# Performance work log

Measured on AMD Instinct MI355X. Metric: run time of the kernel, lower is better.

Reference implementation:

```python
import jax, jax.numpy as jnp
import numpy as np


def gcn_layer(x, src, dst, deg_inv_sqrt, W, b):
    # PyG GCNConv: h = X W; out[i] = sum_{j->i} norm(j,i) * h[j] + deg_i^{-1} * h[i] + b
    n = x.shape[0]
    h = x @ W                                   # [N, out]
    norm = deg_inv_sqrt[src] * deg_inv_sqrt[dst]  # [E]
    msg = h[src] * norm[:, None]                # [E, out]
    agg = jax.ops.segment_sum(msg, dst, num_segments=n)
    # self-loop contribution (added loops with norm = deg_i^{-1})
    agg = agg + h * (deg_inv_sqrt * deg_inv_sqrt)[:, None]
    return agg + b


def setup_inputs() -> dict:
    key = jax.random.key(0)
    k1, k2, k3, k4, k5, k6 = jax.random.split(key, 6)
    N, E, IN, HID, OUT = 50000, 800000, 128, 128, 64
    x = jax.random.normal(k1, (N, IN), dtype=jnp.float32)
    edge_index = jax.random.randint(k2, (2, E), 0, N, dtype=jnp.int64)
    # glorot-ish init for weights, zeros-ish bias
    W1 = jax.random.normal(k3, (IN, HID), dtype=jnp.float32) * (1.0 / np.sqrt(IN))
    b1 = jax.random.normal(k4, (HID,), dtype=jnp.float32) * 0.01
    W2 = jax.random.normal(k5, (HID, OUT), dtype=jnp.float32) * (1.0 / np.sqrt(HID))
    b2 = jax.random.normal(k6, (OUT,), dtype=jnp.float32) * 0.01
    return {"x": x, "edge_index": edge_index, "W1": W1, "b1": b1, "W2": W2, "b2": b2}


def reference(x, edge_index, W1, b1, W2, b2):
    n = x.shape[0]
    src, dst = edge_index[0], edge_index[1]
    # degree with self-loops (PyG computes degree on the dst/col index)
    deg = jax.ops.segment_sum(jnp.ones_like(dst, dtype=x.dtype), dst, num_segments=n) + 1.0
    deg_inv_sqrt = jax.lax.rsqrt(deg)
    h = gcn_layer(x, src, dst, deg_inv_sqrt, W1, b1)
    h = jax.nn.relu(h)
    # F.dropout with training=False is identity (module evaluated in eval mode)
    out = gcn_layer(h, src, dst, deg_inv_sqrt, W2, b2)
    return out
```

## Files before the change

kernel.cpp:

```cpp
#include <hip/hip_runtime.h>
#include <stdint.h>

typedef __attribute__((ext_vector_type(8))) short short8;
typedef __attribute__((ext_vector_type(4))) float floatx4;

static inline size_t align256(size_t x) { return (x + 255) & ~size_t(255); }

__device__ __forceinline__ unsigned short f2bf(float f) {
    unsigned u = __float_as_uint(f);
    u += 0x7fff + ((u >> 16) & 1);
    return (unsigned short)(u >> 16);
}
__device__ __forceinline__ unsigned pack_bf16(float a, float b) {
    return (unsigned)f2bf(a) | ((unsigned)f2bf(b) << 16);
}
__device__ __forceinline__ float bf_lo(unsigned u) { return __uint_as_float(u << 16); }
__device__ __forceinline__ float bf_hi(unsigned u) { return __uint_as_float(u & 0xffff0000u); }

#define BSHIFT 7
#define NBMAX 1024
#define CH 2048
#define SCAP 3072

__device__ __forceinline__ bool detect_i32(const void* eidx, int E, int t) {
    const long long* e64 = (const long long*)eidx;
    int nchk = E < 256 ? E : 256;
    long long v = e64[t % nchk];
    int bad = (v < 0 || v > 0x7fffffffLL) ? 1 : 0;
    return __syncthreads_or(bad) != 0;
}

__global__ __launch_bounds__(256) void k_hist(const void* __restrict__ eidx, int E,
        int* __restrict__ chist, int NB, int NC,
        const float* __restrict__ W1, const float* __restrict__ W2,
        unsigned short* __restrict__ w1t, unsigned short* __restrict__ w2t,
        int K1, int M1, int K2, int M2) {
    __shared__ int hist[NBMAX];
    const int t = threadIdx.x, B = blockIdx.x;
    if (B < NC) {
        const int e0 = B * CH;
        const int e1 = (e0 + CH < E) ? e0 + CH : E;
        const bool i32 = detect_i32(eidx, E, t);
        const int* e32 = (const int*)eidx;
        const long long* e64 = (const long long*)eidx;
        for (int b0 = 0; b0 < NB; b0 += NBMAX) {
            int bw = (NB - b0 < NBMAX) ? NB - b0 : NBMAX;
            for (int i = t; i < bw; i += 256) hist[i] = 0;
            __syncthreads();
            for (int e = e0 + t; e < e1; e += 256) {
                int d = i32 ? e32[(size_t)E + e] : (int)e64[(size_t)E + e];
                int b = (d >> BSHIFT) - b0;
                if (b >= 0 && b < bw) atomicAdd(&hist[b], 1);
            }
            __syncthreads();
            for (int i = t; i < bw; i += 256) chist[(size_t)(b0 + i) * NC + B] = hist[i];
            __syncthreads();
        }
    } else if (B == NC) {
        for (int j = t; j < K1 * M1; j += 256) {
            int k = j / M1, n = j % M1;
            w1t[(size_t)n * K1 + k] = f2bf(W1[j]);
        }
    } else if (B == NC + 1) {
        for (int j = t; j < K2 * M2; j += 256) {
            int k = j / M2, n = j % M2;
            w2t[(size_t)n * K2 + k] = f2bf(W2[j]);
        }
    }
}

__global__ __launch_bounds__(256) void k_btot(const int* __restrict__ chist,
                                              int* __restrict__ btot, int NB, int NC) {
    int b = blockIdx.x * 4 + (threadIdx.x >> 6);
    if (b >= NB) return;
    int lane = threadIdx.x & 63;
    const int* row = chist + (size_t)b * NC;
    int v = 0;
    for (int i = lane; i < NC; i += 64) v += row[i];
    #pragma unroll
    for (int off = 32; off >= 1; off >>= 1) v += __shfl_xor(v, off, 64);
    if (lane == 0) btot[b] = v;
}

__global__ __launch_bounds__(1024) void k_bscan(const int* __restrict__ btot,
                                                int* __restrict__ bbase,
                                                int* __restrict__ rs_final,
                                                int NB, int N) {
    __shared__ int swt[16];
    const int t = threadIdx.x, lane = t & 63, w = t >> 6;
    int carry = 0;
    for (int base = 0; base < NB; base += 1024) {
        int i = base + t;
        int v = (i < NB) ? btot[i] : 0;
        int incl = v;
        #pragma unroll
        for (int off = 1; off < 64; off <<= 1) {
            int nbr = __shfl_up(incl, off, 64);
            if (lane >= off) incl += nbr;
        }
        if (lane == 63) swt[w] = incl;
        __syncthreads();
        int woff = 0;
        for (int j = 0; j < w; ++j) woff += swt[j];
        if (i < NB) bbase[i] = carry + woff + incl - v;
        int tot = 0;
        for (int j = 0; j < 16; ++j) tot += swt[j];
        carry += tot;
        __syncthreads();
    }
    if (t == 0) { bbase[NB] = carry; rs_final[N] = carry; }
}

__global__ __launch_bounds__(256) void k_hscan2(int* __restrict__ chist,
                                                const int* __restrict__ bbase,
                                                int NB, int NC) {
    int b = blockIdx.x * 4 + (threadIdx.x >> 6);
    if (b >= NB) return;
    int lane = threadIdx.x & 63;
    int* row = chist + (size_t)b * NC;
    int carry = bbase[b];
    for (int base = 0; base < NC; base += 64) {
        int i = base + lane;
        int v = (i < NC) ? row[i] : 0;
        int incl = v;
        #pragma unroll
        for (int off = 1; off < 64; off <<= 1) {
            int nbr = __shfl_up(incl, off, 64);
            if (lane >= off) incl += nbr;
        }
        if (i < NC) row[i] = carry + incl - v;
        carry += __shfl(incl, 63, 64);
    }
}

__global__ __launch_bounds__(256) void k_bfill(const void* __restrict__ eidx, int E,
                                               const int* __restrict__ chist,
                                               unsigned* __restrict__ bbuf, int NB, int NC) {
    __shared__ int rank[NBMAX];
    __shared__ int base[NBMAX];
    const int t = threadIdx.x, c = blockIdx.x;
    const int e0 = c * CH;
    const int e1 = (e0 + CH < E) ? e0 + CH : E;
    const bool i32 = detect_i32(eidx, E, t);
    const int* e32 = (const int*)eidx;
    const long long* e64 = (const long long*)eidx;
    for (int b0 = 0; b0 < NB; b0 += NBMAX) {
        int bw = (NB - b0 < NBMAX) ? NB - b0 : NBMAX;
        for (int i = t; i < bw; i += 256) {
            rank[i] = 0;
            base[i] = chist[(size_t)(b0 + i) * NC + c];
        }
        __syncthreads();
        for (int e = e0 + t; e < e1; e += 256) {
            int s, d;
            if (i32) { s = e32[e]; d = e32[(size_t)E + e]; }
            else     { s = (int)e64[e]; d = (int)e64[(size_t)E + e]; }
            int b = (d >> BSHIFT) - b0;
            if (b >= 0 && b < bw) {
                int slot = base[b] + atomicAdd(&rank[b], 1);
                bbuf[slot] = ((unsigned)(d & 127) << 25) | (unsigned)s;
            }
        }
        __syncthreads();
    }
}

__global__ __launch_bounds__(256) void k_sort(const unsigned* __restrict__ bbuf,
                                              const int* __restrict__ bbase,
                                              int* __restrict__ rs_final,
                                              float* __restrict__ dinv,
                                              int* __restrict__ esrc, int N) {
    __shared__ int hist[128];
    __shared__ int off[128];
    __shared__ int srcbuf[SCAP];
    const int b = blockIdx.x, t = threadIdx.x;
    const int node0 = b << BSHIFT;
    const int nloc = (N - node0 < 128) ? N - node0 : 128;
    const int s0 = bbase[b], s1 = bbase[b + 1];
    const int cnt = s1 - s0;
    if (t < 128) hist[t] = 0;
    __syncthreads();
    for (int i = s0 + t; i < s1; i += 256)
        atomicAdd(&hist[bbuf[i] >> 25], 1);
    __syncthreads();
    if (t < 64) {
        int carry = 0;
        #pragma unroll
        for (int base = 0; base < 128; base += 64) {
            int v = hist[base + t];
            int incl = v;
            #pragma unroll
            for (int o = 1; o < 64; o <<= 1) {
                int nbr = __shfl_up(incl, o, 64);
                if (t >= o) incl += nbr;
            }
            off[base + t] = carry + incl - v;
            carry += __shfl(incl, 63, 64);
        }
    }
    __syncthreads();
    if (t < nloc) {
        rs_final[node0 + t] = s0 + off[t];
        dinv[node0 + t] = rsqrtf((float)hist[t] + 1.0f);
    }
    __syncthreads();
    if (t < 128) hist[t] = 0;
    __syncthreads();
    if (cnt <= SCAP) {
        for (int i = s0 + t; i < s1; i += 256) {
            unsigned sd = bbuf[i];
            int lo = sd >> 25;
            int r = atomicAdd(&hist[lo], 1);
            srcbuf[off[lo] + r] = (int)(sd & 0x1ffffffu);
        }
        __syncthreads();
        for (int i = t; i < cnt; i += 256) esrc[s0 + i] = srcbuf[i];
    } else {
        for (int i = s0 + t; i < s1; i += 256) {
            unsigned sd = bbuf[i];
            int lo = sd >> 25;
            int r = atomicAdd(&hist[lo], 1);
            esrc[s0 + off[lo] + r] = (int)(sd & 0x1ffffffu);
        }
    }
}

template<int BN, bool AF32>
__global__ __launch_bounds__(256, 3) void k_gemm(
        const void* __restrict__ Av, const unsigned short* __restrict__ Bt,
        const float* __restrict__ dinv, unsigned short* __restrict__ C,
        int N, int M) {
    constexpr int LD = 136;
    __shared__ unsigned short As[64 * LD];
    __shared__ unsigned short Bs[BN * LD];
    const int tid = threadIdx.x;
    const int wave = tid >> 6, lane = tid & 63;
    const int q = lane >> 4, tm = lane & 15;
    const int row0 = blockIdx.x * 64;

    {
        const uint4* Bg = (const uint4*)Bt;
        #pragma unroll
        for (int it = 0; it < BN / 16; ++it) {
            int i = tid + it * 256;
            int r = i >> 4, o = i & 15;
            *(uint4*)&Bs[r * LD + o * 8] = Bg[(size_t)r * 16 + o];
        }
    }
    if (AF32) {
        const float4* Ag = (const float4*)Av;
        #pragma unroll
        for (int it = 0; it < 8; ++it) {
            int i = tid + it * 256;
            int r = i >> 5, o = i & 31;
            int row = row0 + r;
            float4 v = make_float4(0.f, 0.f, 0.f, 0.f);
            if (row < N) v = Ag[(size_t)row * 32 + o];
            uint2 pk;
            pk.x = pack_bf16(v.x, v.y);
            pk.y = pack_bf16(v.z, v.w);
            *(uint2*)&As[r * LD + o * 4] = pk;
        }
    } else {
        const uint4* Ag = (const uint4*)Av;
        #pragma unroll
        for (int it = 0; it < 4; ++it) {
            int i = tid + it * 256;
            int r = i >> 4, o = i & 15;
            int row = row0 + r;
            uint4 v = make_uint4(0, 0, 0, 0);
            if (row < N) v = Ag[(size_t)row * 16 + o];
            *(uint4*)&As[r * LD + o * 8] = v;
        }
    }
    __syncthreads();

    constexpr int NG = BN / 16;
    floatx4 acc[NG];
    #pragma unroll
    for (int g = 0; g < NG; ++g) acc[g] = (floatx4){0.f, 0.f, 0.f, 0.f};

    const int arow = wave * 16 + tm;
    #pragma unroll
    for (int kc = 0; kc < 4; ++kc) {
        short8 af = *(const short8*)&As[arow * LD + kc * 32 + q * 8];
        #pragma unroll
        for (int g = 0; g < NG; ++g) {
            short8 bf = *(const short8*)&Bs[(g * 16 + tm) * LD + kc * 32 + q * 8];
            acc[g] = __builtin_amdgcn_mfma_f32_16x16x32_bf16(af, bf, acc[g], 0, 0, 0);
        }
    }

    float dv[4];
    #pragma unroll
    for (int r = 0; r < 4; ++r) {
        int row = row0 + wave * 16 + q * 4 + r;
        dv[r] = (row < N) ? dinv[row] : 0.f;
    }
    #pragma unroll
    for (int g = 0; g < NG; ++g) {
        #pragma unroll
        for (int r = 0; r < 4; ++r) {
            int row = row0 + wave * 16 + q * 4 + r;
            if (row < N) C[(size_t)row * M + g * 16 + tm] = f2bf(dv[r] * acc[g][r]);
        }
    }
}

__global__ __launch_bounds__(256) void k_agg128(const unsigned* __restrict__ Hb,
        const float* __restrict__ dinv, const int* __restrict__ rs,
        const int* __restrict__ esrc, const float* __restrict__ bias,
        unsigned* __restrict__ out, int N) {
    int wid = (blockIdx.x * 256 + threadIdx.x) >> 6;
    if (wid >= N) return;
    int l = threadIdx.x & 63;
    float di = dinv[wid];
    unsigned a = Hb[(size_t)wid * 64 + l];
    float accx = bf_lo(a), accy = bf_hi(a);
    int k = rs[wid], kend = rs[wid + 1];
    for (; k + 8 <= kend; k += 8) {
        int s[8];
        #pragma unroll
        for (int j = 0; j < 8; ++j) s[j] = esrc[k + j];
        unsigned g[8];
        #pragma unroll
        for (int j = 0; j < 8; ++j) g[j] = Hb[(size_t)s[j] * 64 + l];
        #pragma unroll
        for (int j = 0; j < 8; ++j) { accx += bf_lo(g[j]); accy += bf_hi(g[j]); }
    }
    if (k + 4 <= kend) {
        int s[4];
        #pragma unroll
        for (int j = 0; j < 4; ++j) s[j] = esrc[k + j];
        unsigned g[4];
        #pragma unroll
        for (int j = 0; j < 4; ++j) g[j] = Hb[(size_t)s[j] * 64 + l];
        #pragma unroll
        for (int j = 0; j < 4; ++j) { accx += bf_lo(g[j]); accy += bf_hi(g[j]); }
        k += 4;
    }
    for (; k < kend; ++k) {
        unsigned g = Hb[(size_t)esrc[k] * 64 + l];
        accx += bf_lo(g); accy += bf_hi(g);
    }
    float2 b = ((const float2*)bias)[l];
    float ox = fmaxf(fmaf(di, accx, b.x), 0.f);
    float oy = fmaxf(fmaf(di, accy, b.y), 0.f);
    out[(size_t)wid * 64 + l] = pack_bf16(ox, oy);
}

__global__ __launch_bounds__(256) void k_agg64(const unsigned short* __restrict__ Hb,
        const float* __restrict__ dinv, const int* __restrict__ rs,
        const int* __restrict__ esrc, const float* __restrict__ bias,
        float* __restrict__ out, int N) {
    int wid = (blockIdx.x * 256 + threadIdx.x) >> 6;
    if (wid >= N) return;
    int l = threadIdx.x & 63;
    float di = dinv[wid];
    float acc = __uint_as_float((unsigned)Hb[(size_t)wid * 64 + l] << 16);
    int k = rs[wid], kend = rs[wid + 1];
    for (; k + 8 <= kend; k += 8) {
        int s[8];
        #pragma unroll
        for (int j = 0; j < 8; ++j) s[j] = esrc[k + j];
        unsigned short g[8];
        #pragma unroll
        for (int j = 0; j < 8; ++j) g[j] = Hb[(size_t)s[j] * 64 + l];
        #pragma unroll
        for (int j = 0; j < 8; ++j) acc += __uint_as_float((unsigned)g[j] << 16);
    }
    if (k + 4 <= kend) {
        int s[4];
        #pragma unroll
        for (int j = 0; j < 4; ++j) s[j] = esrc[k + j];
        unsigned short g[4];
        #pragma unroll
        for (int j = 0; j < 4; ++j) g[j] = Hb[(size_t)s[j] * 64 + l];
        #pragma unroll
        for (int j = 0; j < 4; ++j) acc += __uint_as_float((unsigned)g[j] << 16);
        k += 4;
    }
    for (; k < kend; ++k)
        acc += __uint_as_float((unsigned)Hb[(size_t)esrc[k] * 64 + l] << 16);
    out[(size_t)wid * 64 + l] = fmaf(di, acc, bias[l]);
}

extern "C" void kernel_launch(void* const* d_in, const int* in_sizes, int n_in,
                              void* d_out, int out_size, void* d_ws, size_t ws_size,
                              hipStream_t stream) {
    const float* x  = (const float*)d_in[0];
    const void*  ei = d_in[1];
    const float* W1 = (const float*)d_in[2];
    const float* b1 = (const float*)d_in[3];
    const float* W2 = (const float*)d_in[4];
    const float* b2 = (const float*)d_in[5];

    int HID = in_sizes[3];
    int IN  = in_sizes[2] / HID;
    int OUT = in_sizes[4] / HID;
    int N   = in_sizes[0] / IN;
    int E   = in_sizes[1] / 2;
    int NB  = (N + 127) >> BSHIFT;
    int NC  = (E + CH - 1) / CH;

    char* p = (char*)d_ws;
    int* chist     = (int*)p;   p += align256((size_t)NB * NC * 4);
    int* btot      = (int*)p;   p += align256((size_t)NB * 4);
    int* bbase     = (int*)p;   p += align256((size_t)(NB + 1) * 4);
    int* rs_final  = (int*)p;   p += align256((size_t)(N + 1) * 4);
    int* esrc      = (int*)p;   p += align256((size_t)E * 4);
    float* dinv    = (float*)p; p += align256((size_t)N * 4);
    unsigned short* w1t = (unsigned short*)p; p += align256((size_t)HID * IN * 2);
    unsigned short* w2t = (unsigned short*)p; p += align256((size_t)OUT * HID * 2);
    size_t hb_bytes = (size_t)N * HID * 2, bbuf_bytes = (size_t)E * 4;
    unsigned* bbuf = (unsigned*)p;
    unsigned short* hb = (unsigned short*)p;
    p += align256(hb_bytes > bbuf_bytes ? hb_bytes : bbuf_bytes);
    unsigned short* h1b = (unsigned short*)p; p += align256((size_t)N * HID * 2);
    unsigned short* h2b = (unsigned short*)p; p += align256((size_t)N * OUT * 2);

    k_hist<<<NC + 2, 256, 0, stream>>>(ei, E, chist, NB, NC,
                                       W1, W2, w1t, w2t, IN, HID, HID, OUT);
    k_btot<<<(NB + 3) / 4, 256, 0, stream>>>(chist, btot, NB, NC);
    k_bscan<<<1, 1024, 0, stream>>>(btot, bbase, rs_final, NB, N);
    k_hscan2<<<(NB + 3) / 4, 256, 0, stream>>>(chist, bbase, NB, NC);
    k_bfill<<<NC, 256, 0, stream>>>(ei, E, chist, bbuf, NB, NC);
    k_sort<<<NB, 256, 0, stream>>>(bbuf, bbase, rs_final, dinv, esrc, N);

    k_gemm<128, true><<<(N + 63) / 64, 256, 0, stream>>>(x, w1t, dinv, hb, N, HID);
    k_agg128<<<(N + 3) / 4, 256, 0, stream>>>((unsigned*)hb, dinv, rs_final, esrc, b1,
                                              (unsigned*)h1b, N);

    k_gemm<64, false><<<(N + 63) / 64, 256, 0, stream>>>(h1b, w2t, dinv, h2b, N, OUT);
    k_agg64<<<(N + 3) / 4, 256, 0, stream>>>(h2b, dinv, rs_final, esrc, b2, (float*)d_out, N);
}
```

Before: 208.8 us.

## Vectorize aggregation gathers with 16-byte loads and split edges across lane groups

Both aggregation kernels now have each lane load a uint4 (8 bf16 values) per neighbor row. Each wave is split into groups of lanes that handle different edges at the same time, and the partial sums are combined with xor-shuffle reductions at the end. Edge indices are read cooperatively, 64 at a time, and handed out with shuffles instead of per-lane scalar loads. This aims to cut gather instruction count and raise memory-level parallelism, at the cost of extra shuffle reductions and idle lanes in the final write.

```diff
diff --git a/kernel.cpp b/kernel.cpp
--- a/kernel.cpp
+++ b/kernel.cpp
@@ -307,82 +307,153 @@
     }
 }
 
-__global__ __launch_bounds__(256) void k_agg128(const unsigned* __restrict__ Hb,
+#define ACC8(v) do { \
+    a0 += bf_lo((v).x); a1 += bf_hi((v).x); \
+    a2 += bf_lo((v).y); a3 += bf_hi((v).y); \
+    a4 += bf_lo((v).z); a5 += bf_hi((v).z); \
+    a6 += bf_lo((v).w); a7 += bf_hi((v).w); } while (0)
+
+__global__ __launch_bounds__(256) void k_agg128(const uint4* __restrict__ H4,
         const float* __restrict__ dinv, const int* __restrict__ rs,
         const int* __restrict__ esrc, const float* __restrict__ bias,
-        unsigned* __restrict__ out, int N) {
+        uint4* __restrict__ out, int N) {
     int wid = (blockIdx.x * 256 + threadIdx.x) >> 6;
     if (wid >= N) return;
     int l = threadIdx.x & 63;
-    float di = dinv[wid];
-    unsigned a = Hb[(size_t)wid * 64 + l];
-    float accx = bf_lo(a), accy = bf_hi(a);
-    int k = rs[wid], kend = rs[wid + 1];
-    for (; k + 8 <= kend; k += 8) {
-        int s[8];
-        #pragma unroll
-        for (int j = 0; j < 8; ++j) s[j] = esrc[k + j];
-        unsigned g[8];
-        #pragma unroll
-        for (int j = 0; j < 8; ++j) g[j] = Hb[(size_t)s[j] * 64 + l];
-        #pragma unroll
-        for (int j = 0; j < 8; ++j) { accx += bf_lo(g[j]); accy += bf_hi(g[j]); }
-    }
-    if (k + 4 <= kend) {
-        int s[4];
-        #pragma unroll
-        for (int j = 0; j < 4; ++j) s[j] = esrc[k + j];
-        unsigned g[4];
-        #pragma unroll
-        for (int j = 0; j < 4; ++j) g[j] = Hb[(size_t)s[j] * 64 + l];
-        #pragma unroll
-        for (int j = 0; j < 4; ++j) { accx += bf_lo(g[j]); accy += bf_hi(g[j]); }
-        k += 4;
-    }
-    for (; k < kend; ++k) {
-        unsigned g = Hb[(size_t)esrc[k] * 64 + l];
-        accx += bf_lo(g); accy += bf_hi(g);
-    }
-    float2 b = ((const float2*)bias)[l];
-    float ox = fmaxf(fmaf(di, accx, b.x), 0.f);
-    float oy = fmaxf(fmaf(di, accy, b.y), 0.f);
-    out[(size_t)wid * 64 + l] = pack_bf16(ox, oy);
-}
-
-__global__ __launch_bounds__(256) void k_agg64(const unsigned short* __restrict__ Hb,
+    int g = l >> 4;
+    int q = l & 15;
+    float a0 = 0.f, a1 = 0.f, a2 = 0.f, a3 = 0.f;
+    float a4 = 0.f, a5 = 0.f, a6 = 0.f, a7 = 0.f;
+    int k0 = rs[wid], kend = rs[wid + 1];
+    for (int base = k0; base < kend; base += 64) {
+        int rem = kend - base; if (rem > 64) rem = 64;
+        int idx = esrc[base + (l < rem ? l : 0)];
+        int e0 = 0;
+        for (; e0 + 16 <= rem; e0 += 16) {
+            int s0 = __shfl(idx, e0 + g, 64);
+            int s1 = __shfl(idx, e0 + 4 + g, 64);
+            int s2 = __shfl(idx, e0 + 8 + g, 64);
+            int s3 = __shfl(idx, e0 + 12 + g, 64);
+            uint4 v0 = H4[(size_t)s0 * 16 + q];
+            uint4 v1 = H4[(size_t)s1 * 16 + q];
+            uint4 v2 = H4[(size_t)s2 * 16 + q];
+            uint4 v3 = H4[(size_t)s3 * 16 + q];
+            ACC8(v0); ACC8(v1); ACC8(v2); ACC8(v3);
+        }
+        for (; e0 + 4 <= rem; e0 += 4) {
+            int s0 = __shfl(idx, e0 + g, 64);
+            uint4 v0 = H4[(size_t)s0 * 16 + q];
+            ACC8(v0);
+        }
+        if (e0 < rem) {
+            int s0 = __shfl(idx, e0 + g, 64);
+            if (e0 + g < rem) {
+                uint4 v0 = H4[(size_t)s0 * 16 + q];
+                ACC8(v0);
+            }
+        }
+    }
+    a0 += __shfl_xor(a0, 16, 64); a1 += __shfl_xor(a1, 16, 64);
+    a2 += __shfl_xor(a2, 16, 64); a3 += __shfl_xor(a3, 16, 64);
+    a4 += __shfl_xor(a4, 16, 64); a5 += __shfl_xor(a5, 16, 64);
+    a6 += __shfl_xor(a6, 16, 64); a7 += __shfl_xor(a7, 16, 64);
+    a0 += __shfl_xor(a0, 32, 64); a1 += __shfl_xor(a1, 32, 64);
+    a2 += __shfl_xor(a2, 32, 64); a3 += __shfl_xor(a3, 32, 64);
+    a4 += __shfl_xor(a4, 32, 64); a5 += __shfl_xor(a5, 32, 64);
+    a6 += __shfl_xor(a6, 32, 64); a7 += __shfl_xor(a7, 32, 64);
+    if (g == 0) {
+        uint4 sv = H4[(size_t)wid * 16 + q];
+        ACC8(sv);
+        float di = dinv[wid];
+        float4 bA = ((const float4*)bias)[q * 2];
+        float4 bB = ((const float4*)bias)[q * 2 + 1];
+        float o0 = fmaxf(fmaf(di, a0, bA.x), 0.f);
+        float o1 = fmaxf(fmaf(di, a1, bA.y), 0.f);
+        float o2 = fmaxf(fmaf(di, a2, bA.z), 0.f);
+        float o3 = fmaxf(fmaf(di, a3, bA.w), 0.f);
+        float o4 = fmaxf(fmaf(di, a4, bB.x), 0.f);
+        float o5 = fmaxf(fmaf(di, a5, bB.y), 0.f);
+        float o6 = fmaxf(fmaf(di, a6, bB.z), 0.f);
+        float o7 = fmaxf(fmaf(di, a7, bB.w), 0.f);
+        uint4 pk;
+        pk.x = pack_bf16(o0, o1);
+        pk.y = pack_bf16(o2, o3);
+        pk.z = pack_bf16(o4, o5);
+        pk.w = pack_bf16(o6, o7);
+        out[(size_t)wid * 16 + q] = pk;
+    }
+}
+
+__global__ __launch_bounds__(256) void k_agg64(const uint4* __restrict__ H4,
         const float* __restrict__ dinv, const int* __restrict__ rs,
         const int* __restrict__ esrc, const float* __restrict__ bias,
-        float* __restrict__ out, int N) {
+        float4* __restrict__ out, int N) {
     int wid = (blockIdx.x * 256 + threadIdx.x) >> 6;
     if (wid >= N) return;
     int l = threadIdx.x & 63;
-    float di = dinv[wid];
-    float acc = __uint_as_float((unsigned)Hb[(size_t)wid * 64 + l] << 16);
-    int k = rs[wid], kend = rs[wid + 1];
-    for (; k + 8 <= kend; k += 8) {
-        int s[8];
-        #pragma unroll
-        for (int j = 0; j < 8; ++j) s[j] = esrc[k + j];
-        unsigned short g[8];
-        #pragma unroll
-        for (int j = 0; j < 8; ++j) g[j] = Hb[(size_t)s[j] * 64 + l];
-        #pragma unroll
-        for (int j = 0; j < 8; ++j) acc += __uint_as_float((unsigned)g[j] << 16);
-    }
-    if (k + 4 <= kend) {
-        int s[4];
-        #pragma unroll
-        for (int j = 0; j < 4; ++j) s[j] = esrc[k + j];
-        unsigned short g[4];
-        #pragma unroll
-        for (int j = 0; j < 4; ++j) g[j] = Hb[(size_t)s[j] * 64 + l];
-        #pragma unroll
-        for (int j = 0; j < 4; ++j) acc += __uint_as_float((unsigned)g[j] << 16);
-        k += 4;
-    }
-    for (; k < kend; ++k)
-        acc += __uint_as_float((unsigned)Hb[(size_t)esrc[k] * 64 + l] << 16);
-    out[(size_t)wid * 64 + l] = fmaf(di, acc, bias[l]);
+    int g = l >> 3;
+    int q = l & 7;
+    float a0 = 0.f, a1 = 0.f, a2 = 0.f, a3 = 0.f;
+    float a4 = 0.f, a5 = 0.f, a6 = 0.f, a7 = 0.f;
+    int k0 = rs[wid], kend = rs[wid + 1];
+    for (int base = k0; base < kend; base += 64) {
+        int rem = kend - base; if (rem > 64) rem = 64;
+        int idx = esrc[base + (l < rem ? l : 0)];
+        int e0 = 0;
+        for (; e0 + 32 <= rem; e0 += 32) {
+            int s0 = __shfl(idx, e0 + g, 64);
+            int s1 = __shfl(idx, e0 + 8 + g, 64);
+            int s2 = __shfl(idx, e0 + 16 + g, 64);
+            int s3 = __shfl(idx, e0 + 24 + g, 64);
+            uint4 v0 = H4[(size_t)s0 * 8 + q];
+            uint4 v1 = H4[(size_t)s1 * 8 + q];
+            uint4 v2 = H4[(size_t)s2 * 8 + q];
+            uint4 v3 = H4[(size_t)s3 * 8 + q];
+            ACC8(v0); ACC8(v1); ACC8(v2); ACC8(v3);
+        }
+        for (; e0 + 8 <= rem; e0 += 8) {
+            int s0 = __shfl(idx, e0 + g, 64);
+            uint4 v0 = H4[(size_t)s0 * 8 + q];
+            ACC8(v0);
+        }
+        if (e0 < rem) {
+            int s0 = __shfl(idx, e0 + g, 64);
+            if (e0 + g < rem) {
+                uint4 v0 = H4[(size_t)s0 * 8 + q];
+                ACC8(v0);
+            }
+        }
+    }
+    a0 += __shfl_xor(a0, 8, 64);  a1 += __shfl_xor(a1, 8, 64);
+    a2 += __shfl_xor(a2, 8, 64);  a3 += __shfl_xor(a3, 8, 64);
+    a4 += __shfl_xor(a4, 8, 64);  a5 += __shfl_xor(a5, 8, 64);
+    a6 += __shfl_xor(a6, 8, 64);  a7 += __shfl_xor(a7, 8, 64);
+    a0 += __shfl_xor(a0, 16, 64); a1 += __shfl_xor(a1, 16, 64);
+    a2 += __shfl_xor(a2, 16, 64); a3 += __shfl_xor(a3, 16, 64);
+    a4 += __shfl_xor(a4, 16, 64); a5 += __shfl_xor(a5, 16, 64);
+    a6 += __shfl_xor(a6, 16, 64); a7 += __shfl_xor(a7, 16, 64);
+    a0 += __shfl_xor(a0, 32, 64); a1 += __shfl_xor(a1, 32, 64);
+    a2 += __shfl_xor(a2, 32, 64); a3 += __shfl_xor(a3, 32, 64);
+    a4 += __shfl_xor(a4, 32, 64); a5 += __shfl_xor(a5, 32, 64);
+    a6 += __shfl_xor(a6, 32, 64); a7 += __shfl_xor(a7, 32, 64);
+    if (g == 0) {
+        uint4 sv = H4[(size_t)wid * 8 + q];
+        ACC8(sv);
+        float di = dinv[wid];
+        float4 bA = ((const float4*)bias)[q * 2];
+        float4 bB = ((const float4*)bias)[q * 2 + 1];
+        float4 oA, oB;
+        oA.x = fmaf(di, a0, bA.x);
+        oA.y = fmaf(di, a1, bA.y);
+        oA.z = fmaf(di, a2, bA.z);
+        oA.w = fmaf(di, a3, bA.w);
+        oB.x = fmaf(di, a4, bB.x);
+        oB.y = fmaf(di, a5, bB.y);
+        oB.z = fmaf(di, a6, bB.z);
+        oB.w = fmaf(di, a7, bB.w);
+        out[(size_t)wid * 16 + q * 2]     = oA;
+        out[(size_t)wid * 16 + q * 2 + 1] = oB;
+    }
 }
 
 extern "C" void kernel_launch(void* const* d_in, const int* in_sizes, int n_in,
@@ -428,9 +499,10 @@
     k_sort<<<NB, 256, 0, stream>>>(bbuf, bbase, rs_final, dinv, esrc, N);
 
     k_gemm<128, true><<<(N + 63) / 64, 256, 0, stream>>>(x, w1t, dinv, hb, N, HID);
-    k_agg128<<<(N + 3) / 4, 256, 0, stream>>>((unsigned*)hb, dinv, rs_final, esrc, b1,
-                                              (unsigned*)h1b, N);
+    k_agg128<<<(N + 3) / 4, 256, 0, stream>>>((const uint4*)hb, dinv, rs_final, esrc,
+                                              b1, (uint4*)h1b, N);
 
     k_gemm<64, false><<<(N + 63) / 64, 256, 0, stream>>>(h1b, w2t, dinv, h2b, N, OUT);
-    k_agg64<<<(N + 3) / 4, 256, 0, stream>>>(h2b, dinv, rs_final, esrc, b2, (float*)d_out, N);
-}
+    k_agg64<<<(N + 3) / 4, 256, 0, stream>>>((const uint4*)h2b, dinv, rs_final, esrc,
+                                             b2, (float4*)d_out, N);
+}
```

New measurement: 201.4 us. -3.5%, faster.
